# Performance work log

Measured on AMD Instinct MI355X. Metric: run time of the kernel, lower is better.

Reference implementation:

```python
import jax, jax.numpy as jnp
import numpy as np

T = 256          # trellis length (steps per sequence)
L = 16           # state bits
K = 2            # code bits per step
V = 2            # weights emitted per step
TLUT_BITS = 10   # LUT index bits
OUT, IN = 4096, 4096
NSEQ = (OUT * IN) // (T * V)      # 32768
CODES_PER_WORD = 32 // K          # 16


def fwht(x):
    """Normalized fast Walsh-Hadamard transform along the last axis (power-of-2)."""
    n = x.shape[-1]
    lead = x.shape[:-1]
    h = 1
    while h < n:
        x = x.reshape(lead + (n // (2 * h), 2, h))
        a, b = x[..., 0, :], x[..., 1, :]
        x = jnp.stack([a + b, a - b], axis=-2).reshape(lead + (n,))
        h *= 2
    return x / jnp.sqrt(jnp.asarray(n, x.dtype))


def decode_trellis(trellis, tlut):
    """Bit-unpack K-bit transition codes, run the L-bit shift-register trellis,
    and look up V weight values per state in the LUT."""
    t = jnp.arange(T)
    words = trellis[:, t // CODES_PER_WORD]            # [NSEQ, T] int32
    shifts = (32 - K) - K * (t % CODES_PER_WORD)       # MSB-first unpack
    codes = (words >> shifts) & (2 ** K - 1)           # [NSEQ, T]

    def step(state, code):
        state = ((state << K) | code) & (2 ** L - 1)
        return state, state

    _, states = jax.lax.scan(step, jnp.zeros(trellis.shape[0], jnp.int32),
                             codes.T.astype(jnp.int32))  # states: [T, NSEQ]
    states = states.T                                   # [NSEQ, T]
    vals = tlut[states & (2 ** TLUT_BITS - 1)]          # [NSEQ, T, V] LUT gather
    return vals.reshape(OUT, IN)


def incoherence_process(w_hat, SU, SV):
    """W = diag(SV) H_out  W_hat  H_in diag(SU)  (random-sign Hadamard)."""
    w = fwht(w_hat)        # Hadamard along in-dim
    w = fwht(w.T).T        # Hadamard along out-dim
    return w * SV[:, None] * SU[None, :]


def setup_inputs() -> dict:
    key = jax.random.key(0)
    ks = jax.random.split(key, 5)
    x = jax.random.normal(ks[0], (8192, IN), jnp.float32)
    trellis = jax.random.randint(ks[1], (NSEQ, 32 * T * K // (32 * 32)) if False else (NSEQ, (T * K) // 32), 0, 2147483647, dtype=jnp.int32)
    tlut = jax.random.normal(ks[2], (2 ** TLUT_BITS, V), jnp.float32)
    SU = jnp.sign(jax.random.normal(ks[3], (IN,), jnp.float32)) * 0.02
    SV = jnp.sign(jax.random.normal(ks[4], (OUT,), jnp.float32)) * 0.02
    return {"x": x, "trellis": trellis, "tlut": tlut, "SU": SU, "SV": SV}


def reference(x, trellis, tlut, SU, SV):
    w_hat = decode_trellis(trellis, tlut)       # [OUT, IN] dequantized weight
    w = incoherence_process(w_hat, SU, SV)      # Hadamard incoherence undo
    return x @ w.T                              # F.linear
```

## Files before the change

### kernel.cpp

```cpp
#include <hip/hip_runtime.h>
#include <hip/hip_bf16.h>
#include <stdint.h>

typedef __bf16 bf16x8 __attribute__((ext_vector_type(8)));
typedef float  f32x4  __attribute__((ext_vector_type(4)));

#define IN_DIM  4096
#define OUT_DIM 4096
#define M_DIM   8192

#define AS1 __attribute__((address_space(1)))
#define AS3 __attribute__((address_space(3)))

static __device__ __forceinline__ void gload_lds16(const void* g, void* l) {
  __builtin_amdgcn_global_load_lds((const AS1 void*)g, (AS3 void*)l, 16, 0, 0);
}
static __device__ __forceinline__ float bf2f(unsigned short u) {
  union { uint32_t i; float f; } c; c.i = (uint32_t)u << 16; return c.f;
}
static __device__ __forceinline__ unsigned short f2bf(float f) {
  __hip_bfloat16 h = __float2bfloat16(f); return *(const unsigned short*)&h;
}

__global__ __launch_bounds__(256) void k_decode_fwht_row(
    const int* __restrict__ trellis, const float2* __restrict__ tlut,
    const float* __restrict__ SU, __hip_bfloat16* __restrict__ w,
    const float* __restrict__ x, __hip_bfloat16* __restrict__ xb)
{
  __shared__ float buf[4096];
  __shared__ int words[128];
  __shared__ float2 lut[1024];
  const int tid = threadIdx.x;
  const int r = blockIdx.x;

  float4 xv[8];
  #pragma unroll
  for (int rep = 0; rep < 4; ++rep) {
    size_t i = (((size_t)r * 4 + rep) * 256 + tid) * 8;
    xv[rep * 2]     = *(const float4*)(x + i);
    xv[rep * 2 + 1] = *(const float4*)(x + i + 4);
  }

  if (tid < 128) words[tid] = trellis[r * 128 + tid];
  for (int i = tid; i < 1024; i += 256) lut[i] = tlut[i];
  __syncthreads();

  {
    const int t  = tid;
    const int wi = t >> 4;
    const int sh = 30 - 2 * (t & 15);
    const unsigned mask = (t < 4) ? ((1u << (2 * t + 2)) - 1u) : 1023u;
    #pragma unroll
    for (int s = 0; s < 8; ++s) {
      unsigned lo = (unsigned)words[s * 16 + wi];
      unsigned hi = wi ? (unsigned)words[s * 16 + wi - 1] : 0u;
      unsigned long long comb = ((unsigned long long)hi << 32) | (unsigned long long)lo;
      unsigned st = ((unsigned)(comb >> sh)) & mask;
      float2 v = lut[st];
      buf[s * 512 + 2 * t]     = v.x + v.y;
      buf[s * 512 + 2 * t + 1] = v.x - v.y;
    }
  }
  __syncthreads();

  for (int h = 2; h < 4096; h <<= 1) {
    #pragma unroll
    for (int q = 0; q < 8; ++q) {
      int b = q * 256 + tid;
      int i = ((b & ~(h - 1)) << 1) | (b & (h - 1));
      float a = buf[i], c = buf[i + h];
      buf[i]     = a + c;
      buf[i + h] = a - c;
    }
    __syncthreads();
  }

  for (int it2 = 0; it2 < 2; ++it2) {
    int c0 = (it2 * 256 + tid) * 8;
    union { unsigned short us[8]; uint4 v; } p;
    #pragma unroll
    for (int e = 0; e < 8; ++e)
      p.us[e] = f2bf(buf[c0 + e] * SU[c0 + e] * 0.015625f);
    *(uint4*)(w + (size_t)r * IN_DIM + c0) = p.v;
  }

  #pragma unroll
  for (int rep = 0; rep < 4; ++rep) {
    size_t i = (((size_t)r * 4 + rep) * 256 + tid) * 8;
    float4 v0 = xv[rep * 2], v1 = xv[rep * 2 + 1];
    union { __hip_bfloat16 h[8]; uint4 u; } p;
    p.h[0] = __float2bfloat16(v0.x); p.h[1] = __float2bfloat16(v0.y);
    p.h[2] = __float2bfloat16(v0.z); p.h[3] = __float2bfloat16(v0.w);
    p.h[4] = __float2bfloat16(v1.x); p.h[5] = __float2bfloat16(v1.y);
    p.h[6] = __float2bfloat16(v1.z); p.h[7] = __float2bfloat16(v1.w);
    *(uint4*)(xb + i) = p.u;
  }
}

__global__ __launch_bounds__(256) void k_fwht64_lo(__hip_bfloat16* __restrict__ w)
{
  __shared__ float tile[64][65];
  const int tid = threadIdx.x;
  const int rb = blockIdx.y, cb = blockIdx.x;

  for (int it = 0; it < 2; ++it) {
    int chunk = it * 256 + tid;
    int rr = chunk >> 3, jc = chunk & 7;
    uint4 v = *(const uint4*)(w + (size_t)(rb * 64 + rr) * IN_DIM + cb * 64 + jc * 8);
    const unsigned short* u = (const unsigned short*)&v;
    #pragma unroll
    for (int e = 0; e < 8; ++e) tile[rr][jc * 8 + e] = bf2f(u[e]);
  }
  __syncthreads();

  const int c = tid & 63, qf = tid >> 6;
  for (int h = 1; h < 64; h <<= 1) {
    #pragma unroll
    for (int u = 0; u < 8; ++u) {
      int b = qf * 8 + u;
      int i = ((b & ~(h - 1)) << 1) | (b & (h - 1));
      float a = tile[i][c], d = tile[i + h][c];
      tile[i][c]     = a + d;
      tile[i + h][c] = a - d;
    }
    __syncthreads();
  }

  for (int it = 0; it < 2; ++it) {
    int chunk = it * 256 + tid;
    int rr = chunk >> 3, jc = chunk & 7;
    union { unsigned short us[8]; uint4 v; } p;
    #pragma unroll
    for (int e = 0; e < 8; ++e) p.us[e] = f2bf(tile[rr][jc * 8 + e]);
    *(uint4*)(w + (size_t)(rb * 64 + rr) * IN_DIM + cb * 64 + jc * 8) = p.v;
  }
}

__global__ __launch_bounds__(256) void k_fwht64_hi(__hip_bfloat16* __restrict__ w,
                                                   const float* __restrict__ SV)
{
  __shared__ float tile[64][65];
  const int tid = threadIdx.x;
  const int r0 = blockIdx.y, cb = blockIdx.x;

  for (int it = 0; it < 2; ++it) {
    int chunk = it * 256 + tid;
    int r1 = chunk >> 3, jc = chunk & 7;
    uint4 v = *(const uint4*)(w + (size_t)(r0 + 64 * r1) * IN_DIM + cb * 64 + jc * 8);
    const unsigned short* u = (const unsigned short*)&v;
    #pragma unroll
    for (int e = 0; e < 8; ++e) tile[r1][jc * 8 + e] = bf2f(u[e]);
  }
  __syncthreads();

  const int c = tid & 63, qf = tid >> 6;
  for (int h = 1; h < 64; h <<= 1) {
    #pragma unroll
    for (int u = 0; u < 8; ++u) {
      int b = qf * 8 + u;
      int i = ((b & ~(h - 1)) << 1) | (b & (h - 1));
      float a = tile[i][c], d = tile[i + h][c];
      tile[i][c]     = a + d;
      tile[i + h][c] = a - d;
    }
    __syncthreads();
  }

  for (int it = 0; it < 2; ++it) {
    int chunk = it * 256 + tid;
    int r1 = chunk >> 3, jc = chunk & 7;
    int row = r0 + 64 * r1;
    float sv = SV[row] * 0.015625f;
    union { unsigned short us[8]; uint4 v; } p;
    #pragma unroll
    for (int e = 0; e < 8; ++e) p.us[e] = f2bf(tile[r1][jc * 8 + e] * sv);
    *(uint4*)(w + (size_t)row * IN_DIM + cb * 64 + jc * 8) = p.v;
  }
}

#define GBM 256
#define GBN 256
#define GBK 32
#define NT  (IN_DIM / GBK)

__global__ __launch_bounds__(512, 2) void k_gemm256(
    const __hip_bfloat16* __restrict__ X,
    const __hip_bfloat16* __restrict__ W,
    float* __restrict__ out)
{
  extern __shared__ __hip_bfloat16 smem[];
  __hip_bfloat16* As = smem;
  __hip_bfloat16* Bs = smem + 2 * 8192;

  const int tid  = threadIdx.x;
  const int lane = tid & 63;
  const int wave = tid >> 6;
  const int wm   = wave >> 2;
  const int wn   = wave & 3;
  const int lm   = lane & 15;
  const int lq   = lane >> 4;

  const int nwg  = gridDim.x * gridDim.y;
  const int cpx  = nwg >> 3;
  const int orig = blockIdx.y * gridDim.x + blockIdx.x;
  const int swz  = (orig & 7) * cpx + (orig >> 3);
  const int bx   = swz % gridDim.x;
  const int by   = swz / gridDim.x;
  const int m0 = by * GBM, n0 = bx * GBN;

  f32x4 acc[8][4] = {};

#define STAGE4(buf, kt) do {                                                  \
    _Pragma("unroll")                                                         \
    for (int u_ = 0; u_ < 2; ++u_) {                                          \
      int s_    = u_ * 512 + tid;                                             \
      int line_ = s_ >> 3, pos_ = s_ & 7;                                     \
      int tmp_  = pos_ ^ (line_ & 7);                                         \
      int row_  = line_ * 2 + (tmp_ >> 2);                                    \
      int jc_   = tmp_ & 3;                                                   \
      gload_lds16(X + (size_t)(m0 + row_) * IN_DIM + (kt) * GBK + jc_ * 8,    \
                  As + (buf) * 8192 + s_ * 8);                                \
      gload_lds16(W + (size_t)(n0 + row_) * IN_DIM + (kt) * GBK + jc_ * 8,    \
                  Bs + (buf) * 8192 + s_ * 8);                                \
    }                                                                         \
  } while (0)

#define RD_ALL(FA, FB, BUF) do {                                              \
    const __hip_bfloat16* Ab_ = As + (BUF) * 8192;                            \
    const __hip_bfloat16* Bb_ = Bs + (BUF) * 8192;                            \
    _Pragma("unroll")                                                         \
    for (int mi2 = 0; mi2 < 8; ++mi2) {                                       \
      int r_ = wm * 128 + mi2 * 16 + lm;                                      \
      int ln_ = r_ >> 1;                                                      \
      int po_ = (((r_ & 1) << 2) | lq) ^ (ln_ & 7);                           \
      FA[mi2] = *(const bf16x8*)(Ab_ + ln_ * 64 + po_ * 8);                   \
    }                                                                         \
    _Pragma("unroll")                                                         \
    for (int ni2 = 0; ni2 < 4; ++ni2) {                                       \
      int r_ = wn * 64 + ni2 * 16 + lm;                                       \
      int ln_ = r_ >> 1;                                                      \
      int po_ = (((r_ & 1) << 2) | lq) ^ (ln_ & 7);                           \
      FB[ni2] = *(const bf16x8*)(Bb_ + ln_ * 64 + po_ * 8);                   \
    }                                                                         \
  } while (0)

#define MFMA_ALL(FA, FB) do {                                                 \
    _Pragma("unroll")                                                         \
    for (int mi2 = 0; mi2 < 8; ++mi2)                                         \
      _Pragma("unroll")                                                       \
      for (int ni2 = 0; ni2 < 4; ++ni2)                                       \
        acc[mi2][ni2] = __builtin_amdgcn_mfma_f32_16x16x32_bf16(              \
            FA[mi2], FB[ni2], acc[mi2][ni2], 0, 0, 0);                        \
  } while (0)

#define FENCE asm volatile("" ::: "memory")
#define BAR do { FENCE; __builtin_amdgcn_s_barrier(); FENCE; } while (0)
#define DRAIN_ALL do { asm volatile("s_waitcnt vmcnt(0) lgkmcnt(0)" ::: "memory"); } while (0)

  bf16x8 fa0[8], fb0[4], fa1[8], fb1[4];

  STAGE4(0, 0);
  STAGE4(1, 1);
  DRAIN_ALL;
  BAR;
  RD_ALL(fa0, fb0, 0);
  asm volatile("s_waitcnt lgkmcnt(0)" ::: "memory");
  BAR;

  for (int it = 0; it < NT / 2; ++it) {
    const int t2 = (2 * it + 2 < NT) ? 2 * it + 2 : NT - 1;
    const int t3 = (2 * it + 3 < NT) ? 2 * it + 3 : NT - 1;

    STAGE4(0, t2);
    RD_ALL(fa1, fb1, 1);
    __builtin_amdgcn_s_setprio(1);
    MFMA_ALL(fa0, fb0);
    __builtin_amdgcn_s_setprio(0);
    DRAIN_ALL;
    BAR;

    STAGE4(1, t3);
    RD_ALL(fa0, fb0, 0);
    __builtin_amdgcn_s_setprio(1);
    MFMA_ALL(fa1, fb1);
    __builtin_amdgcn_s_setprio(0);
    DRAIN_ALL;
    BAR;
  }

  #pragma unroll
  for (int mi = 0; mi < 8; ++mi) {
    #pragma unroll
    for (int ni = 0; ni < 4; ++ni) {
      int col   = n0 + wn * 64 + ni * 16 + lm;
      int rbase = m0 + wm * 128 + mi * 16 + lq * 4;
      #pragma unroll
      for (int rg = 0; rg < 4; ++rg) {
        out[(size_t)(rbase + rg) * OUT_DIM + col] = acc[mi][ni][rg];
      }
    }
  }
#undef DRAIN_ALL
#undef BAR
#undef FENCE
#undef MFMA_ALL
#undef RD_ALL
#undef STAGE4
}

extern "C" void kernel_launch(void* const* d_in, const int* in_sizes, int n_in,
                              void* d_out, int out_size, void* d_ws, size_t ws_size,
                              hipStream_t stream) {
  (void)in_sizes; (void)n_in; (void)out_size; (void)ws_size;
  const float* x       = (const float*)d_in[0];
  const int*   trellis = (const int*)d_in[1];
  const float* tlut    = (const float*)d_in[2];
  const float* SU      = (const float*)d_in[3];
  const float* SV      = (const float*)d_in[4];
  float* out = (float*)d_out;

  __hip_bfloat16* Wd = (__hip_bfloat16*)d_ws;
  __hip_bfloat16* Xb = (__hip_bfloat16*)((char*)d_ws + (size_t)32 * 1024 * 1024);

  k_decode_fwht_row<<<4096, 256, 0, stream>>>(trellis, (const float2*)tlut, SU, Wd, x, Xb);
  k_fwht64_lo<<<dim3(64, 64), 256, 0, stream>>>(Wd);
  k_fwht64_hi<<<dim3(64, 64), 256, 0, stream>>>(Wd, SV);

  hipFuncSetAttribute((const void*)k_gemm256,
                      hipFuncAttributeMaxDynamicSharedMemorySize, 65536);
  k_gemm256<<<dim3(IN_DIM / GBN, M_DIM / GBM), 512, 65536, stream>>>(Xb, Wd, out);
}
```

Before: 347.5 us.

## Triple-buffer GEMM LDS stages with partial vmcnt waits instead of full drains

```diff
diff --git a/kernel.cpp b/kernel.cpp
--- a/kernel.cpp
+++ b/kernel.cpp
@@ -190,7 +190,7 @@
 {
   extern __shared__ __hip_bfloat16 smem[];
   __hip_bfloat16* As = smem;
-  __hip_bfloat16* Bs = smem + 2 * 8192;
+  __hip_bfloat16* Bs = smem + 3 * 8192;
 
   const int tid  = threadIdx.x;
   const int lane = tid & 63;
@@ -255,38 +255,45 @@
 
 #define FENCE asm volatile("" ::: "memory")
 #define BAR do { FENCE; __builtin_amdgcn_s_barrier(); FENCE; } while (0)
-#define DRAIN_ALL do { asm volatile("s_waitcnt vmcnt(0) lgkmcnt(0)" ::: "memory"); } while (0)
+#define PH_WAIT do { asm volatile("s_waitcnt vmcnt(4) lgkmcnt(0)" ::: "memory"); } while (0)
+
+#define PHASE(SB, RB, FCA, FCB, FRA, FRB, T) do {                             \
+    int ts_ = ((T) + 3 < NT) ? (T) + 3 : NT - 1;                              \
+    STAGE4(SB, ts_);                                                          \
+    RD_ALL(FRA, FRB, RB);                                                     \
+    __builtin_amdgcn_s_setprio(1);                                            \
+    MFMA_ALL(FCA, FCB);                                                       \
+    __builtin_amdgcn_s_setprio(0);                                            \
+    PH_WAIT;                                                                  \
+    BAR;                                                                      \
+  } while (0)
 
   bf16x8 fa0[8], fb0[4], fa1[8], fb1[4];
 
   STAGE4(0, 0);
   STAGE4(1, 1);
-  DRAIN_ALL;
+  STAGE4(2, 2);
+  asm volatile("s_waitcnt vmcnt(8)" ::: "memory");
   BAR;
   RD_ALL(fa0, fb0, 0);
-  asm volatile("s_waitcnt lgkmcnt(0)" ::: "memory");
+  asm volatile("s_waitcnt vmcnt(4) lgkmcnt(0)" ::: "memory");
   BAR;
 
-  for (int it = 0; it < NT / 2; ++it) {
-    const int t2 = (2 * it + 2 < NT) ? 2 * it + 2 : NT - 1;
-    const int t3 = (2 * it + 3 < NT) ? 2 * it + 3 : NT - 1;
-
-    STAGE4(0, t2);
-    RD_ALL(fa1, fb1, 1);
-    __builtin_amdgcn_s_setprio(1);
-    MFMA_ALL(fa0, fb0);
-    __builtin_amdgcn_s_setprio(0);
-    DRAIN_ALL;
-    BAR;
-
-    STAGE4(1, t3);
-    RD_ALL(fa0, fb0, 0);
-    __builtin_amdgcn_s_setprio(1);
-    MFMA_ALL(fa1, fb1);
-    __builtin_amdgcn_s_setprio(0);
-    DRAIN_ALL;
-    BAR;
-  }
+  for (int it = 0; it < 21; ++it) {
+    const int t = 6 * it;
+    PHASE(0, 1, fa0, fb0, fa1, fb1, t);
+    PHASE(1, 2, fa1, fb1, fa0, fb0, t + 1);
+    PHASE(2, 0, fa0, fb0, fa1, fb1, t + 2);
+    PHASE(0, 1, fa1, fb1, fa0, fb0, t + 3);
+    PHASE(1, 2, fa0, fb0, fa1, fb1, t + 4);
+    PHASE(2, 0, fa1, fb1, fa0, fb0, t + 5);
+  }
+
+  PHASE(0, 1, fa0, fb0, fa1, fb1, 126);
+  __builtin_amdgcn_s_setprio(1);
+  MFMA_ALL(fa1, fb1);
+  __builtin_amdgcn_s_setprio(0);
+  asm volatile("s_waitcnt vmcnt(0)" ::: "memory");
 
   #pragma unroll
   for (int mi = 0; mi < 8; ++mi) {
@@ -300,7 +307,8 @@
       }
     }
   }
-#undef DRAIN_ALL
+#undef PHASE
+#undef PH_WAIT
 #undef BAR
 #undef FENCE
 #undef MFMA_ALL
@@ -327,6 +335,6 @@
   k_fwht64_hi<<<dim3(64, 64), 256, 0, stream>>>(Wd, SV);
 
   hipFuncSetAttribute((const void*)k_gemm256,
-                      hipFuncAttributeMaxDynamicSharedMemorySize, 65536);
-  k_gemm256<<<dim3(IN_DIM / GBN, M_DIM / GBM), 512, 65536, stream>>>(Xb, Wd, out);
-}
+                      hipFuncAttributeMaxDynamicSharedMemorySize, 98304);
+  k_gemm256<<<dim3(IN_DIM / GBN, M_DIM / GBM), 512, 98304, stream>>>(Xb, Wd, out);
+}
```

New measurement: 510.2 us. 46.8% more time.
